# Kernel optimization log

Hardware: AMD Instinct MI355X
Metric: run time of the kernel (lower is better)

The kernel has to match this reference:

```python
import jax, jax.numpy as jnp
import numpy as np

N = 100000      # num_nodes
E = 600000      # edges per relation
R = 3           # num_relations
F_IN = 128
F_OUT = 64


def setup_inputs() -> dict:
    key = jax.random.key(0)
    k0, k1, k2, k3 = jax.random.split(key, 4)
    x = jax.random.normal(k0, (N, F_IN), dtype=jnp.float32)
    edge_indices = jax.random.randint(k1, (R, 2, E), 0, N, dtype=jnp.int32)
    # torch.randperm per relation -> fixed permutations as int inputs
    perms = jnp.stack([jax.random.permutation(jax.random.fold_in(k2, r), N).astype(jnp.int32)
                       for r in range(R)])
    # GCNConv glorot weight + zero bias, one per relation
    Ws = jax.random.normal(k3, (R, F_IN, F_OUT), dtype=jnp.float32) * (1.0 / np.sqrt(F_IN))
    bs = jnp.zeros((R, F_OUT), dtype=jnp.float32)
    return {"x": x, "edge_indices": edge_indices, "perms": perms, "Ws": Ws, "bs": bs}


def gcn_conv(h, src, dst, W, b, n):
    """PyG GCNConv: add self-loops, sym-normalize, linear, scatter-sum, bias."""
    loops = jnp.arange(n, dtype=src.dtype)
    s = jnp.concatenate([src, loops])
    d = jnp.concatenate([dst, loops])
    deg = jax.ops.segment_sum(jnp.ones_like(s, dtype=h.dtype), d, num_segments=n)
    dinv = jnp.where(deg > 0, jax.lax.rsqrt(deg), 0.0)
    norm = dinv[s] * dinv[d]                      # [E+n]
    hw = h @ W                                    # [n, F_OUT]
    out = jax.ops.segment_sum(hw[s] * norm[:, None], d, num_segments=n)
    return out + b


def reference(x, edge_indices, perms, Ws, bs):
    # Eval mode: F.dropout(p=0.5, training=False) is identity.
    n = x.shape[0]
    pos_hs, neg_hs, summaries = [], [], []
    for r in range(R):
        src, dst = edge_indices[r, 0], edge_indices[r, 1]
        pos_h = jax.nn.relu(gcn_conv(x, src, dst, Ws[r], bs[r], n))
        neg_h = jax.nn.relu(gcn_conv(x[perms[r]], src, dst, Ws[r], bs[r], n))
        pos_hs.append(pos_h)
        neg_hs.append(neg_h)
        summaries.append(pos_h.mean(axis=0, keepdims=True))
    return (jnp.stack(pos_hs), jnp.stack(neg_hs), jnp.stack(summaries))
```

## Files before the change

### kernel.cpp

```cpp
#include <hip/hip_runtime.h>

#define F_IN 128
#define F_OUT 64
#define CAP 32

typedef float f32x2 __attribute__((ext_vector_type(2)));
typedef float f32x4 __attribute__((ext_vector_type(4)));
typedef short bf16x8 __attribute__((ext_vector_type(8)));

__device__ __forceinline__ unsigned short f2bf(float f) {
    unsigned int u = __float_as_uint(f);
    u += 0x7fff + ((u >> 16) & 1);
    return (unsigned short)(u >> 16);
}
__device__ __forceinline__ float bf2f(unsigned short s) {
    return __uint_as_float((unsigned int)s << 16);
}

__global__ __launch_bounds__(256) void prep_kernel(const int* __restrict__ ei,
                                                   const int* __restrict__ perm,
                                                   const float* __restrict__ W,
                                                   int* __restrict__ deg,
                                                   int* __restrict__ csr,
                                                   int* __restrict__ ip,
                                                   unsigned short* __restrict__ wt_hi,
                                                   unsigned short* __restrict__ wt_lo,
                                                   int N, int E, int R,
                                                   int degB, int invB) {
    int b = blockIdx.x;
    if (b < degB) {
        int idx = b * 256 + threadIdx.x;
        if (idx < R * E) {
            int r = idx / E, e = idx - r * E;
            const int* base = ei + (size_t)r * 2 * E;
            int s = base[e], d = base[E + e];
            int pos = atomicAdd(&deg[(size_t)r * N + d], 1) & (CAP - 1);
            csr[((size_t)r * N + d) * CAP + pos] = s;
        }
    } else if (b < degB + invB) {
        int idx = (b - degB) * 256 + threadIdx.x;
        if (idx < R * N) {
            int r = idx / N, i = idx - r * N;
            ip[(size_t)r * N + perm[idx]] = i;
        }
    } else {
        int idx = (b - degB - invB) * 256 + threadIdx.x;
        if (idx < R * 64 * 128) {
            int k = idx & 127, c = (idx >> 7) & 63, r = idx >> 13;
            float v = W[((size_t)r * F_IN + k) * F_OUT + c];
            unsigned short h = f2bf(v);
            wt_hi[idx] = h;
            wt_lo[idx] = f2bf(v - bf2f(h));
        }
    }
}

__global__ __launch_bounds__(256) void gemm_xw(const float* __restrict__ x,
                                               const unsigned short* __restrict__ wt_hi,
                                               const unsigned short* __restrict__ wt_lo,
                                               const int* __restrict__ ip,
                                               const int* __restrict__ deg,
                                               unsigned short* __restrict__ combined,
                                               int N, int R) {
    constexpr int KP = 136;
    __shared__ __align__(16) unsigned short xs_hi[64 * KP];
    __shared__ __align__(16) unsigned short xs_lo[64 * KP];

    int row0 = blockIdx.x * 64;
    int tid = threadIdx.x;
    {
        int rr = tid >> 2, q = tid & 3;
        int grow = row0 + rr; if (grow >= N) grow = N - 1;
        const float* xr = x + (size_t)grow * F_IN + q * 32;
        unsigned short* dh = &xs_hi[rr * KP + q * 32];
        unsigned short* dl = &xs_lo[rr * KP + q * 32];
        #pragma unroll
        for (int c = 0; c < 32; c += 4) {
            float4 v = *(const float4*)(xr + c);
            unsigned short h0 = f2bf(v.x), h1 = f2bf(v.y),
                           h2 = f2bf(v.z), h3 = f2bf(v.w);
            ushort4 hv; hv.x = h0; hv.y = h1; hv.z = h2; hv.w = h3;
            *(ushort4*)(dh + c) = hv;
            ushort4 lv;
            lv.x = f2bf(v.x - bf2f(h0)); lv.y = f2bf(v.y - bf2f(h1));
            lv.z = f2bf(v.z - bf2f(h2)); lv.w = f2bf(v.w - bf2f(h3));
            *(ushort4*)(dl + c) = lv;
        }
    }
    __syncthreads();

    int wv = tid >> 6, lane = tid & 63;
    int l15 = lane & 15, lhi = lane >> 4;
    int nbase = wv * 16;
    int xrow = row0 + nbase + l15;
    for (int r = 0; r < R; ++r) {
        f32x4 acc[4];
        #pragma unroll
        for (int ct = 0; ct < 4; ++ct) acc[ct] = (f32x4){0.f, 0.f, 0.f, 0.f};
        const unsigned short* wh = wt_hi + (size_t)r * 64 * 128;
        const unsigned short* wl = wt_lo + (size_t)r * 64 * 128;
        #pragma unroll
        for (int kc = 0; kc < 4; ++kc) {
            int kb = kc * 32 + lhi * 8;
            int ro = (nbase + l15) * KP + kb;
            bf16x8 bh = *(const bf16x8*)&xs_hi[ro];
            bf16x8 bl = *(const bf16x8*)&xs_lo[ro];
            #pragma unroll
            for (int ct = 0; ct < 4; ++ct) {
                int wo = (ct * 16 + l15) * 128 + kb;
                bf16x8 ah = *(const bf16x8*)(wh + wo);
                bf16x8 al = *(const bf16x8*)(wl + wo);
                acc[ct] = __builtin_amdgcn_mfma_f32_16x16x32_bf16(ah, bh, acc[ct], 0, 0, 0);
                acc[ct] = __builtin_amdgcn_mfma_f32_16x16x32_bf16(ah, bl, acc[ct], 0, 0, 0);
                acc[ct] = __builtin_amdgcn_mfma_f32_16x16x32_bf16(al, bh, acc[ct], 0, 0, 0);
            }
        }
        if (xrow < N) {
            size_t rb = (size_t)r * N;
            int t = ip[rb + xrow];
            float dvp = rsqrtf((float)(deg[rb + xrow] + 1));
            float dvn = rsqrtf((float)(deg[rb + t] + 1));
            #pragma unroll
            for (int ct = 0; ct < 4; ++ct) {
                f32x4 a = acc[ct];
                int cb = ct * 16 + lhi * 4;
                ushort4 vp;
                vp.x = f2bf(a.x * dvp); vp.y = f2bf(a.y * dvp);
                vp.z = f2bf(a.z * dvp); vp.w = f2bf(a.w * dvp);
                *(ushort4*)(combined + (rb + xrow) * 128 + cb) = vp;
                ushort4 vn;
                vn.x = f2bf(a.x * dvn); vn.y = f2bf(a.y * dvn);
                vn.z = f2bf(a.z * dvn); vn.w = f2bf(a.w * dvn);
                *(ushort4*)(combined + (rb + t) * 128 + 64 + cb) = vn;
            }
        }
    }
}

__global__ __launch_bounds__(256) void gather_kernel(const int* __restrict__ csr,
                                                     const int* __restrict__ deg,
                                                     const unsigned short* __restrict__ combined,
                                                     const float* __restrict__ bs,
                                                     float* __restrict__ out_pos,
                                                     float* __restrict__ out_neg,
                                                     float* __restrict__ partial,
                                                     int N, int perRel) {
    int bid = blockIdx.x;
    int r = bid / perRel, ib = bid - r * perRel;
    int lane = threadIdx.x & 63, wv = threadIdx.x >> 6;
    int i = __builtin_amdgcn_readfirstlane(ib * 4 + wv);
    int c0 = (lane & 31) * 2;
    __shared__ float ls[4][64];
    float p0 = 0.f, p1 = 0.f;
    if (i < N) {
        const unsigned short* cw = combined + (size_t)r * N * 128;
        const int* cs = csr + (size_t)r * N * CAP;
        int d = __builtin_amdgcn_readfirstlane(deg[(size_t)r * N + i]);
        int dd = min(d, CAP);
        float dv = rsqrtf((float)(d + 1));
        unsigned int sv = *(const unsigned int*)(cw + (size_t)i * 128 + 2 * lane);
        float acc0 = bf2f((unsigned short)sv);
        float acc1 = bf2f((unsigned short)(sv >> 16));
        size_t rowb = (size_t)i * CAP;
        int last = dd - 1;
        for (int j = 0; j < dd; j += 8) {
            int s8[8]; float m8[8];
            #pragma unroll
            for (int k = 0; k < 8; ++k) {
                int idx = j + k;
                int ic = idx < last ? idx : last;
                s8[k] = cs[rowb + ic];
                m8[k] = (idx < dd) ? 1.f : 0.f;
            }
            #pragma unroll
            for (int k = 0; k < 8; ++k) {
                unsigned int v = *(const unsigned int*)(cw + (size_t)s8[k] * 128 + 2 * lane);
                acc0 += bf2f((unsigned short)v) * m8[k];
                acc1 += bf2f((unsigned short)(v >> 16)) * m8[k];
            }
        }
        float2 bv = *(const float2*)(bs + r * F_OUT + c0);
        float q0 = acc0 * dv + bv.x; q0 = q0 > 0.f ? q0 : 0.f;
        float q1 = acc1 * dv + bv.y; q1 = q1 > 0.f ? q1 : 0.f;
        size_t off = (size_t)r * N * F_OUT + (size_t)i * F_OUT + c0;
        float* dst = (lane < 32) ? (out_pos + off) : (out_neg + off);
        f32x2 o; o.x = q0; o.y = q1;
        __builtin_nontemporal_store(o, (f32x2*)dst);
        if (lane < 32) { p0 = q0; p1 = q1; }
    }
    if (lane < 32) { ls[wv][c0] = p0; ls[wv][c0 + 1] = p1; }
    __syncthreads();
    if (wv == 0) {
        float t = ls[0][lane] + ls[1][lane] + ls[2][lane] + ls[3][lane];
        atomicAdd(&partial[((size_t)r * 256 + (ib & 255)) * F_OUT + lane], t);
    }
}

__global__ __launch_bounds__(256) void summary_reduce(const float* __restrict__ partial,
                                                      float* __restrict__ summary,
                                                      float inv_n) {
    int r = blockIdx.x;
    int lane = threadIdx.x & 63, wv = threadIdx.x >> 6;
    __shared__ float ls[256];
    float s = 0.f;
    for (int c = wv; c < 256; c += 4)
        s += partial[((size_t)r * 256 + c) * F_OUT + lane];
    ls[threadIdx.x] = s;
    __syncthreads();
    if (wv == 0)
        summary[r * F_OUT + lane] =
            (ls[lane] + ls[64 + lane] + ls[128 + lane] + ls[192 + lane]) * inv_n;
}

extern "C" void kernel_launch(void* const* d_in, const int* in_sizes, int n_in,
                              void* d_out, int out_size, void* d_ws, size_t ws_size,
                              hipStream_t stream) {
    const float* x    = (const float*)d_in[0];
    const int*   ei   = (const int*)d_in[1];
    const int*   perm = (const int*)d_in[2];
    const float* Ws   = (const float*)d_in[3];
    const float* bs   = (const float*)d_in[4];

    const int N = in_sizes[0] / F_IN;
    const int R = in_sizes[4] / F_OUT;
    const int E = in_sizes[1] / (2 * R);

    float* out_pos = (float*)d_out;
    float* out_neg = out_pos + (size_t)R * N * F_OUT;
    float* summary = out_neg + (size_t)R * N * F_OUT;

    char* ws = (char*)d_ws;
    size_t off = 0;
    auto alloc = [&](size_t bytes) { void* p = ws + off;
        off += (bytes + 255) & ~(size_t)255; return p; };
    int*   deg      = (int*)  alloc((size_t)R * N * 4);
    float* partial  = (float*)alloc((size_t)R * 256 * F_OUT * 4);
    int*   csr      = (int*)  alloc((size_t)R * N * CAP * 4);
    int*   ip       = (int*)  alloc((size_t)R * N * 4);
    unsigned short* combined = (unsigned short*)alloc((size_t)R * N * 128 * 2);
    unsigned short* wt_hi = (unsigned short*)alloc((size_t)R * 64 * 128 * 2);
    unsigned short* wt_lo = (unsigned short*)alloc((size_t)R * 64 * 128 * 2);

    const int degB = (R * E + 255) / 256;
    const int invB = (R * N + 255) / 256;
    const int wB   = (R * 64 * 128 + 255) / 256;
    const int gemmB = (N + 63) / 64;
    const int perRel = (N + 3) / 4;

    size_t zbytes = (size_t)((char*)csr - (char*)deg);
    hipMemsetAsync(deg, 0, zbytes, stream);

    prep_kernel<<<degB + invB + wB, 256, 0, stream>>>(ei, perm, Ws, deg, csr, ip,
                                                      wt_hi, wt_lo, N, E, R,
                                                      degB, invB);
    gemm_xw<<<gemmB, 256, 0, stream>>>(x, wt_hi, wt_lo, ip, deg, combined, N, R);
    gather_kernel<<<perRel * R, 256, 0, stream>>>(csr, deg, combined, bs,
                                                  out_pos, out_neg, partial,
                                                  N, perRel);
    summary_reduce<<<R, 256, 0, stream>>>(partial, summary, 1.0f / (float)N);
}
```

Before: 570.2 us.

## Partition edge scatter by destination range per XCD to localize atomics

```diff
diff --git a/kernel.cpp b/kernel.cpp
--- a/kernel.cpp
+++ b/kernel.cpp
@@ -26,25 +26,35 @@
                                                    unsigned short* __restrict__ wt_hi,
                                                    unsigned short* __restrict__ wt_lo,
                                                    int N, int E, int R,
-                                                   int degB, int invB) {
+                                                   int edgeB, int invB) {
     int b = blockIdx.x;
-    if (b < degB) {
-        int idx = b * 256 + threadIdx.x;
-        if (idx < R * E) {
-            int r = idx / E, e = idx - r * E;
-            const int* base = ei + (size_t)r * 2 * E;
-            int s = base[e], d = base[E + e];
-            int pos = atomicAdd(&deg[(size_t)r * N + d], 1) & (CAP - 1);
-            csr[((size_t)r * N + d) * CAP + pos] = s;
-        }
-    } else if (b < degB + invB) {
-        int idx = (b - degB) * 256 + threadIdx.x;
+    if (b < edgeB) {
+        int xcd = b & 7, chunk = b >> 3;
+        int lo = (int)(((long long)xcd * N) >> 3);
+        int hi = (int)(((long long)(xcd + 1) * N) >> 3);
+        int base = chunk * 1024 + threadIdx.x;
+        #pragma unroll
+        for (int k = 0; k < 4; ++k) {
+            int idx = base + k * 256;
+            if (idx < R * E) {
+                int r = idx / E, e = idx - r * E;
+                const int* bb = ei + (size_t)r * 2 * E;
+                int d = bb[E + e];
+                if (d >= lo && d < hi) {
+                    int s = bb[e];
+                    int pos = atomicAdd(&deg[(size_t)r * N + d], 1) & (CAP - 1);
+                    csr[((size_t)r * N + d) * CAP + pos] = s;
+                }
+            }
+        }
+    } else if (b < edgeB + invB) {
+        int idx = (b - edgeB) * 256 + threadIdx.x;
         if (idx < R * N) {
             int r = idx / N, i = idx - r * N;
             ip[(size_t)r * N + perm[idx]] = i;
         }
     } else {
-        int idx = (b - degB - invB) * 256 + threadIdx.x;
+        int idx = (b - edgeB - invB) * 256 + threadIdx.x;
         if (idx < R * 64 * 128) {
             int k = idx & 127, c = (idx >> 7) & 63, r = idx >> 13;
             float v = W[((size_t)r * F_IN + k) * F_OUT + c];
@@ -241,7 +251,7 @@
     unsigned short* wt_hi = (unsigned short*)alloc((size_t)R * 64 * 128 * 2);
     unsigned short* wt_lo = (unsigned short*)alloc((size_t)R * 64 * 128 * 2);
 
-    const int degB = (R * E + 255) / 256;
+    const int edgeB = 8 * ((R * E + 1023) / 1024);
     const int invB = (R * N + 255) / 256;
     const int wB   = (R * 64 * 128 + 255) / 256;
     const int gemmB = (N + 63) / 64;
@@ -250,9 +260,9 @@
     size_t zbytes = (size_t)((char*)csr - (char*)deg);
     hipMemsetAsync(deg, 0, zbytes, stream);
 
-    prep_kernel<<<degB + invB + wB, 256, 0, stream>>>(ei, perm, Ws, deg, csr, ip,
-                                                      wt_hi, wt_lo, N, E, R,
-                                                      degB, invB);
+    prep_kernel<<<edgeB + invB + wB, 256, 0, stream>>>(ei, perm, Ws, deg, csr, ip,
+                                                       wt_hi, wt_lo, N, E, R,
+                                                       edgeB, invB);
     gemm_xw<<<gemmB, 256, 0, stream>>>(x, wt_hi, wt_lo, ip, deg, combined, N, R);
     gather_kernel<<<perRel * R, 256, 0, stream>>>(csr, deg, combined, bs,
                                                   out_pos, out_neg, partial,
```

Result: faster. 510.7 us (-10.4%).
